# Kernel optimization log

Hardware: AMD Instinct MI355X
Metric: run time of the kernel (lower is better)

The kernel has to match this reference:

```python
import jax, jax.numpy as jnp
import numpy as np

B, S = 2, 2048
DIM_IN, DIM_OUT, NUM_HEADS, DIM_QK = 1024, 128, 16, 128


def setup_inputs() -> dict:
    key = jax.random.key(0)
    k0, k1, k2, k3 = jax.random.split(key, 4)
    x = jax.random.normal(k0, (B, S, DIM_IN), jnp.float32)
    mask = jax.random.bernoulli(k1, 0.1, (B, S))  # True = masked-out token
    # xavier-normal-ish scales (exact init values are irrelevant for correctness)
    std_in = float(np.sqrt(2.0 / (NUM_HEADS * DIM_QK + DIM_IN * DIM_QK)))
    proj_in = jax.random.normal(k2, (DIM_IN, NUM_HEADS, 2 * DIM_QK + DIM_OUT), jnp.float32) * std_in
    v_bias = jnp.zeros((NUM_HEADS, DIM_OUT), jnp.float32)
    std_out = float(np.sqrt(2.0 / (DIM_OUT * DIM_OUT + NUM_HEADS * DIM_OUT)))
    proj_out = jax.random.normal(k3, (NUM_HEADS, DIM_OUT, DIM_OUT), jnp.float32) * std_out
    proj_out_bias = jnp.zeros((DIM_OUT,), jnp.float32)
    return {"x": x, "mask": mask, "proj_in": proj_in, "v_bias": v_bias,
            "proj_out": proj_out, "proj_out_bias": proj_out_bias}


def _rotary(t):
    # t: [z, s, h, d]; GPT-NeoX style rotary as in the torch Rotary module
    d = t.shape[-1]
    half = -(-d // 2)  # ceil(d/2), matches torch.arange(0,-1,-2/d)
    freq_half = 10000.0 ** (jnp.arange(half, dtype=jnp.float32) * (-2.0 / d))
    freq = jnp.concatenate([freq_half, freq_half[: half - d % 2]])  # length d
    pos = jnp.arange(t.shape[1], dtype=jnp.float32)
    ang = pos[:, None] * freq[None, :]             # [s, d]
    cos = jnp.cos(ang)[None, :, None, :]
    sin = jnp.sin(ang)[None, :, None, :]
    x1, x2 = jnp.split(t, 2, axis=-1)
    rot = jnp.concatenate([-x2, x1], axis=-1)
    return t * cos + rot * sin


def _inf_cube(t):
    return t ** 3


def reference(x, mask, proj_in, v_bias, proj_out, proj_out_bias):
    qkv = jnp.einsum('zki,iho->zkho', x, proj_in)
    q, k, v = jnp.split(qkv, [DIM_QK, 2 * DIM_QK], axis=-1)
    q = _rotary(q)
    k = _rotary(k)
    scores = jnp.einsum('zqha,zkha->zqkh', q, k) / jnp.sqrt(jnp.float32(DIM_QK))
    # dual mask: row (query) OR column (key) masked -> -inf
    m = jnp.logical_or(mask[:, :, None, None], mask[:, None, :, None])  # [z,q,k,1]
    scores = jnp.where(m, -jnp.inf, scores)
    attn = jnp.nan_to_num(jax.nn.softmax(scores, axis=2))  # softmax over k; nan rows -> 0
    o = jnp.einsum('zqkh,zkhx->zqhx', attn, v + v_bias[None, None])
    out = jnp.einsum('zqhx,hxy->zqy', _inf_cube(o), proj_out) + proj_out_bias[None, None]
    return _inf_cube(out)
```

## Files before the change

kernel.cpp:

```cpp
#include <hip/hip_runtime.h>
#include <math.h>

#define BZ 2
#define SQ 2048
#define DIN 1024
#define HH 16
#define NT 6144
#define MROWS 4096
#define KOUT 2048
#define KSPLIT 16

typedef unsigned short u16t;
typedef unsigned int u32t;
typedef __attribute__((ext_vector_type(8))) short bf16x8;
typedef __attribute__((ext_vector_type(4))) float f32x4;

__device__ __forceinline__ float cubef(float x) { return x * x * x; }

__device__ __forceinline__ u16t f2bf(float f) {
    u32t b = __float_as_uint(f);
    b += 0x7FFFu + ((b >> 16) & 1u);
    return (u16t)(b >> 16);
}
__device__ __forceinline__ float bf2f(u16t u) { return __uint_as_float(((u32t)u) << 16); }
__device__ __forceinline__ u32t pk2(float a, float b) {
    return (u32t)f2bf(a) | ((u32t)f2bf(b) << 16);
}

#if __has_builtin(__builtin_amdgcn_exp2f)
#define EXP2(x) __builtin_amdgcn_exp2f(x)
#else
#define EXP2(x) exp2f(x)
#endif

__device__ __forceinline__ void load_lds16(const void* g, void* l) {
    __builtin_amdgcn_global_load_lds((const __attribute__((address_space(1))) void*)g,
                                     (__attribute__((address_space(3))) void*)l, 16, 0, 0);
}

__global__ __launch_bounds__(256) void bf16_x(const float* __restrict__ x,
                                              u16t* __restrict__ xb) {
    const size_t idx = ((size_t)blockIdx.x * 256 + threadIdx.x) * 8;
    float4 f0 = *(const float4*)&x[idx];
    float4 f1 = *(const float4*)&x[idx + 4];
    u32t h[4];
    h[0] = pk2(f0.x, f0.y); h[1] = pk2(f0.z, f0.w);
    h[2] = pk2(f1.x, f1.y); h[3] = pk2(f1.z, f1.w);
    *(uint4*)&xb[idx] = *(uint4*)&h[0];
}

__global__ __launch_bounds__(256) void rope_table(float* __restrict__ tab) {
    const int idx = blockIdx.x * 256 + threadIdx.x;
    const int s = idx >> 6, d = idx & 63;
    float f = expf(-0.14391156831212788f * (float)d);
    float sn, cs;
    sincosf((float)s * f, &sn, &cs);
    ((float2*)tab)[idx] = make_float2(cs, sn);
}

__global__ __launch_bounds__(256) void transpose_w(const float* __restrict__ W,
                                                   u16t* __restrict__ Th) {
    __shared__ float tile[64][68];
    const int n0 = blockIdx.x * 64;
    const int k0 = blockIdx.y * 64;
    const int t = threadIdx.x;
    {
        const int r = t >> 4, c = (t & 15) * 4;
        #pragma unroll
        for (int p = 0; p < 4; p++) {
            float4 v = *(const float4*)&W[(size_t)(k0 + r + p * 16) * NT + n0 + c];
            *(float4*)&tile[r + p * 16][c] = v;
        }
    }
    __syncthreads();
    const int nr = t >> 2;
    const int kc = (t & 3) * 16;
    u32t hi[8];
    #pragma unroll
    for (int j = 0; j < 8; j++)
        hi[j] = pk2(tile[kc + 2 * j][nr], tile[kc + 2 * j + 1][nr]);
    size_t ob = (size_t)(n0 + nr) * DIN + k0 + kc;
    *(uint4*)&Th[ob]     = *(uint4*)&hi[0];
    *(uint4*)&Th[ob + 8] = *(uint4*)&hi[4];
}

__global__ __launch_bounds__(256) void transpose_w2(const float* __restrict__ W,
                                                    u16t* __restrict__ Th) {
    __shared__ float tile[64][68];
    const int n0 = blockIdx.x * 64;
    const int k0 = blockIdx.y * 64;
    const int t = threadIdx.x;
    {
        const int r = t >> 4, c = (t & 15) * 4;
        #pragma unroll
        for (int p = 0; p < 4; p++) {
            float4 v = *(const float4*)&W[(size_t)(k0 + r + p * 16) * 128 + n0 + c];
            *(float4*)&tile[r + p * 16][c] = v;
        }
    }
    __syncthreads();
    const int nr = t >> 2;
    const int kc = (t & 3) * 16;
    u32t hi[8];
    #pragma unroll
    for (int j = 0; j < 8; j++)
        hi[j] = pk2(tile[kc + 2 * j][nr], tile[kc + 2 * j + 1][nr]);
    size_t ob = (size_t)(n0 + nr) * KOUT + k0 + kc;
    *(uint4*)&Th[ob]     = *(uint4*)&hi[0];
    *(uint4*)&Th[ob + 8] = *(uint4*)&hi[4];
}

#define QSC 0.12751744f

__global__ __launch_bounds__(256) void gemm_qkv5(const u16t* __restrict__ Ah,
                                                 const u16t* __restrict__ Bh,
                                                 const float* __restrict__ vb,
                                                 const float* __restrict__ ropetab,
                                                 u16t* __restrict__ QB,
                                                 u16t* __restrict__ KB,
                                                 u16t* __restrict__ VTh) {
    __shared__ __align__(16) u16t smem[17408];

    const int t = threadIdx.x;
    const int lane = t & 63, wid = t >> 6;
    const int quad = lane >> 4, l15 = lane & 15;
    const int wm = (wid & 1) * 64;
    const int wn = (wid >> 1) * 64;

    const int f = blockIdx.y * 48 + blockIdx.x;
    const int L = (f & 7) * 192 + (f >> 3);
    const int rect = L / 48, rrem = L - rect * 48;
    const int tileI = (rect & 7) * 6 + rrem % 6;
    const int rowIdx = (rect >> 3) * 8 + rrem / 6;
    const int h = tileI / 3, t3 = tileI - h * 3;
    const int colBase = tileI * 128;
    const int rowBase = rowIdx * 128;
    const int sm = t & 127;
    const int skh = t >> 7;

    f32x4 acc[4][4];
    #pragma unroll
    for (int i = 0; i < 4; i++)
        #pragma unroll
        for (int j = 0; j < 4; j++) acc[i][j] = (f32x4){0.f, 0.f, 0.f, 0.f};

    const u16t* aPtr = Ah + (size_t)(rowBase + sm) * DIN + skh * 16;
    const u16t* bPtr = Bh + (size_t)(colBase + sm) * DIN + skh * 16;
    const int wbase = (wid >> 1) * 2048 + (wid & 1) * 512;

    load_lds16(aPtr,     &smem[wbase]);
    load_lds16(aPtr + 8, &smem[wbase + 1024]);
    load_lds16(bPtr,     &smem[8192 + wbase]);
    load_lds16(bPtr + 8, &smem[8192 + wbase + 1024]);
    __syncthreads();

    for (int it = 0; it < 32; it++) {
        const int buf = it & 1;
        const int ab = buf * 4096, bb_ = 8192 + buf * 4096;
        if (it < 31) {
            const int k0 = (it + 1) * 32;
            const int nab = (buf ^ 1) * 4096, nbb = 8192 + (buf ^ 1) * 4096;
            load_lds16(aPtr + k0,     &smem[nab + wbase]);
            load_lds16(aPtr + k0 + 8, &smem[nab + wbase + 1024]);
            load_lds16(bPtr + k0,     &smem[nbb + wbase]);
            load_lds16(bPtr + k0 + 8, &smem[nbb + wbase + 1024]);
        }
        bf16x8 ah[4], bh[4];
        #pragma unroll
        for (int mt = 0; mt < 4; mt++)
            ah[mt] = *(const bf16x8*)&smem[ab + quad * 1024 + (wm + mt * 16 + l15) * 8];
        #pragma unroll
        for (int nt = 0; nt < 4; nt++)
            bh[nt] = *(const bf16x8*)&smem[bb_ + quad * 1024 + (wn + nt * 16 + l15) * 8];
        #pragma unroll
        for (int mt = 0; mt < 4; mt++)
            #pragma unroll
            for (int nt = 0; nt < 4; nt++)
                acc[mt][nt] = __builtin_amdgcn_mfma_f32_16x16x32_bf16(ah[mt], bh[nt], acc[mt][nt], 0, 0, 0);
        __syncthreads();
    }

    const int z = rowBase >> 11;
    const int s0local = rowBase & 2047;
    const size_t zh = (size_t)(z * 16 + h);
    u16t* tl = smem;

    if (t3 == 2) {
        #pragma unroll
        for (int nt = 0; nt < 4; nt++) {
            float bbv = vb[h * 128 + wn + nt * 16 + l15];
            #pragma unroll
            for (int mt = 0; mt < 4; mt++)
                #pragma unroll
                for (int r = 0; r < 4; r++)
                    tl[(wm + mt * 16 + quad * 4 + r) * 136 + wn + nt * 16 + l15] =
                        f2bf(acc[mt][nt][r] + bbv);
        }
    } else {
        #pragma unroll
        for (int nt = 0; nt < 4; nt++)
            #pragma unroll
            for (int mt = 0; mt < 4; mt++)
                #pragma unroll
                for (int r = 0; r < 4; r++)
                    tl[(wm + mt * 16 + quad * 4 + r) * 136 + wn + nt * 16 + l15] =
                        f2bf(acc[mt][nt][r]);
    }
    __syncthreads();

    if (t3 != 2) {
        u16t* dstQK = (t3 ? KB : QB) + zh * 262144;
        const float sc = t3 ? 1.0f : QSC;
        const int rr = t >> 2;
        const int ch = (t & 3) << 4;
        #pragma unroll
        for (int half = 0; half < 2; half++) {
            const int row = rr + half * 64;
            const int s = s0local + row;
            const u16t* trow = &tl[row * 136];
            uint4 X1  = *(const uint4*)&trow[ch];
            uint4 X1b = *(const uint4*)&trow[ch + 8];
            uint4 X2  = *(const uint4*)&trow[ch + 64];
            uint4 X2b = *(const uint4*)&trow[ch + 72];
            u32t A_[8] = {X1.x, X1.y, X1.z, X1.w, X1b.x, X1b.y, X1b.z, X1b.w};
            u32t B_[8] = {X2.x, X2.y, X2.z, X2.w, X2b.x, X2b.y, X2b.z, X2b.w};
            u32t OA[8], OB[8];
            const float4* tb = (const float4*)&ropetab[(size_t)s * 128 + ch * 2];
            #pragma unroll
            for (int p = 0; p < 8; p++) {
                float4 tt = tb[p];
                float cs0 = tt.x * sc, sn0 = tt.y * sc;
                float cs1 = tt.z * sc, sn1 = tt.w * sc;
                float x1a = bf2f((u16t)(A_[p] & 0xFFFFu)), x1b = bf2f((u16t)(A_[p] >> 16));
                float x2a = bf2f((u16t)(B_[p] & 0xFFFFu)), x2b = bf2f((u16t)(B_[p] >> 16));
                OA[p] = pk2(x1a * cs0 - x2a * sn0, x1b * cs1 - x2b * sn1);
                OB[p] = pk2(x2a * cs0 + x1a * sn0, x2b * cs1 + x1b * sn1);
            }
            u16t* d0 = dstQK + (size_t)s * 128 + ch;
            *(uint4*)d0        = make_uint4(OA[0], OA[1], OA[2], OA[3]);
            *(uint4*)(d0 + 8)  = make_uint4(OA[4], OA[5], OA[6], OA[7]);
            *(uint4*)(d0 + 64) = make_uint4(OB[0], OB[1], OB[2], OB[3]);
            *(uint4*)(d0 + 72) = make_uint4(OB[4], OB[5], OB[6], OB[7]);
        }
    } else {
        u16t* dstV = VTh + zh * 262144 + (size_t)(s0local >> 5) * 4096;
        const int d = t & 127;
        const int g0 = t >> 7;
        #pragma unroll
        for (int gg = 0; gg < 2; gg++) {
            const int g = g0 + 2 * gg;
            const u16t* col = &tl[(g * 32) * 136 + d];
            u32t H[16];
            #pragma unroll
            for (int m = 0; m < 16; m++) {
                u32t lo = col[m * 136];
                u32t hi = col[(m + 16) * 136];
                H[m] = lo | (hi << 16);
            }
            u16t* dv = dstV + (size_t)g * 4096 + d * 32;
            *(uint4*)&dv[0]  = *(uint4*)&H[0];
            *(uint4*)&dv[8]  = *(uint4*)&H[4];
            *(uint4*)&dv[16] = *(uint4*)&H[8];
            *(uint4*)&dv[24] = *(uint4*)&H[12];
        }
    }
}

__global__ __launch_bounds__(256, 2) void attn_kernel8(const u16t* __restrict__ QB,
                                                       const u16t* __restrict__ KB,
                                                       const u16t* __restrict__ VTh,
                                                       const int* __restrict__ mask,
                                                       u16t* __restrict__ O3b) {
    const int blk = blockIdx.x;
    const int qt = blk & 15;
    const int h  = (blk >> 4) & 15;
    const int z  = blk >> 8;
    const int t  = threadIdx.x;
    const int lane = t & 63, wid = t >> 6;
    const int quad = lane >> 4, l15 = lane & 15;

    __shared__ __align__(16) u16t ks[2][32 * 136];
    __shared__ __align__(16) u16t vth[2][128 * 40];
    __shared__ __align__(16) u16t wlb[128 * 40];
    __shared__ int km[2][32];

    const int q0 = qt * 128;
    const size_t zh = (size_t)(z * 16 + h);
    const u16t* qb  = QB  + zh * 262144;
    const u16t* kb  = KB  + zh * 262144;
    const u16t* vhg = VTh + zh * 262144;

    bf16x8 qf[2][4];
    #pragma unroll
    for (int i = 0; i < 2; i++)
        #pragma unroll
        for (int kk = 0; kk < 4; kk++)
            qf[i][kk] = *(const bf16x8*)(qb + (size_t)(q0 + 16 * (2 * wid + i) + l15) * 128 + kk * 32 + quad * 8);

    int4 qm4[2];
    #pragma unroll
    for (int i = 0; i < 2; i++)
        qm4[i] = *(const int4*)&mask[z * SQ + q0 + 16 * (2 * wid + i) + 4 * quad];
    const int qmr[2][4] = {{qm4[0].x, qm4[0].y, qm4[0].z, qm4[0].w},
                           {qm4[1].x, qm4[1].y, qm4[1].z, qm4[1].w}};
    int rowoff[2];
    #pragma unroll
    for (int i = 0; i < 2; i++) rowoff[i] = (16 * (2 * wid + i) + 4 * quad) * 40;

    const int srow = t >> 3, sco = (t & 7) * 16;
    const int sdd = t >> 1, sk0 = (t & 1) * 16;

    uint4 ka, kb2, va, vb2;
    int kmv = 0;
    {
        ka  = *(const uint4*)(kb + t * 16);
        kb2 = *(const uint4*)(kb + t * 16 + 8);
        va  = *(const uint4*)(vhg + t * 16);
        vb2 = *(const uint4*)(vhg + t * 16 + 8);
        if (t < 32) kmv = mask[z * SQ + t];
    }

    f32x4 acc[2][8];
    #pragma unroll
    for (int i = 0; i < 2; i++)
        #pragma unroll
        for (int d = 0; d < 8; d++) acc[i][d] = (f32x4){0.f, 0.f, 0.f, 0.f};
    float dsum[2][4] = {{0.f, 0.f, 0.f, 0.f}, {0.f, 0.f, 0.f, 0.f}};

    for (int it = 0; it < 64; it++) {
        const int buf = it & 1;
        *(uint4*)&ks[buf][srow * 136 + sco]     = ka;
        *(uint4*)&ks[buf][srow * 136 + sco + 8] = kb2;
        *(uint4*)&vth[buf][sdd * 40 + sk0]      = va;
        *(uint4*)&vth[buf][sdd * 40 + sk0 + 8]  = vb2;
        if (t < 32) km[buf][t] = kmv;

        __syncthreads();

        {
            const int ktn = (it < 63) ? (it + 1) * 32 : it * 32;
            const u16t* src = kb + (size_t)ktn * 128 + t * 16;
            ka  = *(const uint4*)(src);
            kb2 = *(const uint4*)(src + 8);
            const u16t* srch = vhg + (size_t)(ktn >> 5) * 4096 + t * 16;
            va  = *(const uint4*)(srch);
            vb2 = *(const uint4*)(srch + 8);
            if (t < 32) kmv = mask[z * SQ + ktn + t];
        }

        f32x4 s4[2][2];
        #pragma unroll
        for (int i = 0; i < 2; i++)
            #pragma unroll
            for (int n = 0; n < 2; n++) s4[i][n] = (f32x4){0.f, 0.f, 0.f, 0.f};
        #pragma unroll
        for (int kk = 0; kk < 4; kk++) {
            bf16x8 kf0 = *(const bf16x8*)&ks[buf][l15 * 136 + kk * 32 + quad * 8];
            bf16x8 kf1 = *(const bf16x8*)&ks[buf][(16 + l15) * 136 + kk * 32 + quad * 8];
            s4[0][0] = __builtin_amdgcn_mfma_f32_16x16x32_bf16(qf[0][kk], kf0, s4[0][0], 0, 0, 0);
            s4[0][1] = __builtin_amdgcn_mfma_f32_16x16x32_bf16(qf[0][kk], kf1, s4[0][1], 0, 0, 0);
            s4[1][0] = __builtin_amdgcn_mfma_f32_16x16x32_bf16(qf[1][kk], kf0, s4[1][0], 0, 0, 0);
            s4[1][1] = __builtin_amdgcn_mfma_f32_16x16x32_bf16(qf[1][kk], kf1, s4[1][1], 0, 0, 0);
        }
        {
            int colm0 = km[buf][l15], colm1 = km[buf][16 + l15];
            #pragma unroll
            for (int i = 0; i < 2; i++)
                #pragma unroll
                for (int r = 0; r < 4; r++) {
                    float w0 = (qmr[i][r] | colm0) ? 0.f : EXP2(s4[i][0][r]);
                    float w1 = (qmr[i][r] | colm1) ? 0.f : EXP2(s4[i][1][r]);
                    dsum[i][r] += w0 + w1;
                    u32t pkw;
                    asm("v_cvt_pk_bf16_f32 %0, %1, %2" : "=v"(pkw) : "v"(w0), "v"(w1));
                    *(u32t*)&wlb[rowoff[i] + r * 40 + 2 * l15] = pkw;
                }
        }
        bf16x8 pa[2];
        #pragma unroll
        for (int i = 0; i < 2; i++)
            pa[i] = *(const bf16x8*)&wlb[(16 * (2 * wid + i) + l15) * 40 + quad * 8];
        #pragma unroll
        for (int dt = 0; dt < 8; dt++) {
            bf16x8 vh = *(const bf16x8*)&vth[buf][(16 * dt + l15) * 40 + quad * 8];
            acc[0][dt] = __builtin_amdgcn_mfma_f32_16x16x32_bf16(pa[0], vh, acc[0][dt], 0, 0, 0);
            acc[1][dt] = __builtin_amdgcn_mfma_f32_16x16x32_bf16(pa[1], vh, acc[1][dt], 0, 0, 0);
        }
    }

    #pragma unroll
    for (int i = 0; i < 2; i++)
        #pragma unroll
        for (int r = 0; r < 4; r++) {
            float v = dsum[i][r];
            v += __shfl_xor(v, 1);
            v += __shfl_xor(v, 2);
            v += __shfl_xor(v, 4);
            v += __shfl_xor(v, 8);
            dsum[i][r] = v;
        }

    #pragma unroll
    for (int i = 0; i < 2; i++)
        #pragma unroll
        for (int r = 0; r < 4; r++) {
            int row = 16 * (2 * wid + i) + 4 * quad + r;
            float inv = dsum[i][r] > 0.f ? 1.f / dsum[i][r] : 0.f;
            u16t* dst = O3b + (size_t)(z * SQ + q0 + row) * KOUT + h * 128;
            #pragma unroll
            for (int dt = 0; dt < 8; dt++)
                dst[16 * dt + l15] = f2bf(cubef(acc[i][dt][r] * inv));
        }
}

__global__ __launch_bounds__(256) void final_gemm3(const u16t* __restrict__ Ab,
                                                   const u16t* __restrict__ Bh,
                                                   float* __restrict__ part) {
    __shared__ __align__(16) u16t as_h[2][4 * 128 * 8];
    __shared__ __align__(16) u16t bs_h[2][4 * 128 * 8];

    const int t = threadIdx.x;
    const int lane = t & 63, wid = t >> 6;
    const int quad = lane >> 4, l15 = lane & 15;
    const int wm = (wid & 1) * 64;
    const int wn = (wid >> 1) * 64;
    const int rowBase = blockIdx.x * 128;
    const int kBase   = blockIdx.y * (KOUT / KSPLIT);
    const int sm = t & 127;
    const int skh = t >> 7;

    f32x4 acc[4][4];
    #pragma unroll
    for (int i = 0; i < 4; i++)
        #pragma unroll
        for (int j = 0; j < 4; j++) acc[i][j] = (f32x4){0.f, 0.f, 0.f, 0.f};

    const u16t* aPtr = Ab + (size_t)(rowBase + sm) * KOUT + kBase + skh * 16;
    const u16t* bPtr = Bh + (size_t)sm * KOUT + kBase + skh * 16;
    const int swoff = (skh * 2) * 1024 + sm * 8;

    uint4 a0 = *(const uint4*)(aPtr);
    uint4 a1 = *(const uint4*)(aPtr + 8);
    uint4 b0 = *(const uint4*)(bPtr);
    uint4 b1 = *(const uint4*)(bPtr + 8);

    const int NIT = (KOUT / KSPLIT) / 32;
    for (int it = 0; it < NIT; it++) {
        const int buf = it & 1;
        *(uint4*)(&as_h[buf][swoff])        = a0;
        *(uint4*)(&as_h[buf][swoff + 1024]) = a1;
        *(uint4*)(&bs_h[buf][swoff])        = b0;
        *(uint4*)(&bs_h[buf][swoff + 1024]) = b1;
        __syncthreads();
        {
            const int k0 = (it < NIT - 1) ? (it + 1) * 32 : it * 32;
            a0 = *(const uint4*)(aPtr + k0);
            a1 = *(const uint4*)(aPtr + k0 + 8);
            b0 = *(const uint4*)(bPtr + k0);
            b1 = *(const uint4*)(bPtr + k0 + 8);
        }
        bf16x8 ah[4], bh[4];
        #pragma unroll
        for (int mt = 0; mt < 4; mt++)
            ah[mt] = *(const bf16x8*)&as_h[buf][quad * 1024 + (wm + mt * 16 + l15) * 8];
        #pragma unroll
        for (int nt = 0; nt < 4; nt++)
            bh[nt] = *(const bf16x8*)&bs_h[buf][quad * 1024 + (wn + nt * 16 + l15) * 8];
        #pragma unroll
        for (int mt = 0; mt < 4; mt++)
            #pragma unroll
            for (int nt = 0; nt < 4; nt++)
                acc[mt][nt] = __builtin_amdgcn_mfma_f32_16x16x32_bf16(ah[mt], bh[nt], acc[mt][nt], 0, 0, 0);
    }

    float* pbase = part + (size_t)blockIdx.y * ((size_t)MROWS * 128);
    #pragma unroll
    for (int mt = 0; mt < 4; mt++)
        #pragma unroll
        for (int nt = 0; nt < 4; nt++) {
            int col = wn + nt * 16 + l15;
            #pragma unroll
            for (int r = 0; r < 4; r++) {
                int row = rowBase + wm + mt * 16 + quad * 4 + r;
                pbase[(size_t)row * 128 + col] = acc[mt][nt][r];
            }
        }
}

__global__ __launch_bounds__(256) void reduce_bias_cube(const float* __restrict__ part,
                                                        const float* __restrict__ bias,
                                                        float* __restrict__ out) {
    const int idx = (blockIdx.x * 256 + threadIdx.x) * 4;
    float4 s = {0.f, 0.f, 0.f, 0.f};
    #pragma unroll
    for (int p = 0; p < KSPLIT; p++) {
        float4 v = *(const float4*)&part[(size_t)p * ((size_t)MROWS * 128) + idx];
        s.x += v.x; s.y += v.y; s.z += v.z; s.w += v.w;
    }
    float4 b = *(const float4*)&bias[idx & 127];
    float4 r;
    r.x = cubef(s.x + b.x);
    r.y = cubef(s.y + b.y);
    r.z = cubef(s.z + b.z);
    r.w = cubef(s.w + b.w);
    *(float4*)&out[idx] = r;
}

extern "C" void kernel_launch(void* const* d_in, const int* in_sizes, int n_in,
                              void* d_out, int out_size, void* d_ws, size_t ws_size,
                              hipStream_t stream) {
    const float* x        = (const float*)d_in[0];
    const int*   mask     = (const int*)d_in[1];
    const float* proj_in  = (const float*)d_in[2];
    const float* v_bias   = (const float*)d_in[3];
    const float* proj_out = (const float*)d_in[4];
    const float* po_bias  = (const float*)d_in[5];
    float* out = (float*)d_out;

    u16t* QB  = (u16t*)d_ws;
    u16t* KB  = QB + (size_t)8388608;
    u16t* VTh = KB + (size_t)8388608;
    u16t* xb  = VTh + (size_t)8388608;
    u16t* O3b = xb + (size_t)4194304;
    u16t* pTh = O3b;
    float* ropetab = (float*)(O3b + (size_t)6291456);
    u16t* WTh = QB;
    float* partials = (float*)(WTh + (size_t)128 * KOUT);

    bf16_x<<<(MROWS * DIN) / (256 * 8), 256, 0, stream>>>(x, xb);
    rope_table<<<(SQ * 64) / 256, 256, 0, stream>>>(ropetab);
    transpose_w<<<dim3(NT / 64, DIN / 64), 256, 0, stream>>>(proj_in, pTh);
    gemm_qkv5<<<dim3(48, MROWS / 128), 256, 0, stream>>>(xb, pTh, v_bias, ropetab, QB, KB, VTh);
    attn_kernel8<<<BZ * HH * (SQ / 128), 256, 0, stream>>>(QB, KB, VTh, mask, O3b);
    transpose_w2<<<dim3(2, KOUT / 64), 256, 0, stream>>>(proj_out, WTh);
    final_gemm3<<<dim3(MROWS / 128, KSPLIT), 256, 0, stream>>>(O3b, WTh, partials);
    reduce_bias_cube<<<(MROWS * 128) / (256 * 4), 256, 0, stream>>>(partials, po_bias, out);
}
```

Measured before the change: 310.4 us.

## Deepen GEMM pipelines to 4-stage async LDS loads, add MFMA priority hints

```diff
diff --git a/kernel.cpp b/kernel.cpp
--- a/kernel.cpp
+++ b/kernel.cpp
@@ -8,7 +8,7 @@
 #define NT 6144
 #define MROWS 4096
 #define KOUT 2048
-#define KSPLIT 16
+#define KSPLIT 8
 
 typedef unsigned short u16t;
 typedef unsigned int u32t;
@@ -112,14 +112,47 @@
 
 #define QSC 0.12751744f
 
-__global__ __launch_bounds__(256) void gemm_qkv5(const u16t* __restrict__ Ah,
-                                                 const u16t* __restrict__ Bh,
-                                                 const float* __restrict__ vb,
-                                                 const float* __restrict__ ropetab,
-                                                 u16t* __restrict__ QB,
-                                                 u16t* __restrict__ KB,
-                                                 u16t* __restrict__ VTh) {
-    __shared__ __align__(16) u16t smem[17408];
+#define GQ_STAGE(TI) do {                                                  \
+    const int _k0 = (TI) * 32;                                             \
+    const int _bb = ((TI) & 3) * 8192;                                     \
+    load_lds16(aPtr + _k0,     &smem[_bb + wbase]);                        \
+    load_lds16(aPtr + _k0 + 8, &smem[_bb + wbase + 1024]);                 \
+    load_lds16(bPtr + _k0,     &smem[_bb + 4096 + wbase]);                 \
+    load_lds16(bPtr + _k0 + 8, &smem[_bb + 4096 + wbase + 1024]);          \
+} while (0)
+
+#define GQ_COMPUTE(TI) do {                                                \
+    const int _bb = ((TI) & 3) * 8192;                                     \
+    bf16x8 ah[4], bh[4];                                                   \
+    _Pragma("unroll")                                                      \
+    for (int mt = 0; mt < 4; mt++)                                         \
+        ah[mt] = *(const bf16x8*)&smem[_bb + quad * 1024 + (wm + mt * 16 + l15) * 8]; \
+    _Pragma("unroll")                                                      \
+    for (int nt = 0; nt < 4; nt++)                                         \
+        bh[nt] = *(const bf16x8*)&smem[_bb + 4096 + quad * 1024 + (wn + nt * 16 + l15) * 8]; \
+    __builtin_amdgcn_s_setprio(1);                                         \
+    _Pragma("unroll")                                                      \
+    for (int mt = 0; mt < 4; mt++)                                         \
+        _Pragma("unroll")                                                  \
+        for (int nt = 0; nt < 4; nt++)                                     \
+            acc[mt][nt] = __builtin_amdgcn_mfma_f32_16x16x32_bf16(ah[mt], bh[nt], acc[mt][nt], 0, 0, 0); \
+    __builtin_amdgcn_s_setprio(0);                                         \
+} while (0)
+
+#define GQ_WAITBAR(N) do {                                                 \
+    asm volatile("s_waitcnt vmcnt(" #N ")" ::: "memory");                  \
+    __builtin_amdgcn_s_barrier();                                          \
+    __builtin_amdgcn_sched_barrier(0);                                     \
+} while (0)
+
+__global__ __launch_bounds__(256, 2) void gemm_qkv6(const u16t* __restrict__ Ah,
+                                                    const u16t* __restrict__ Bh,
+                                                    const float* __restrict__ vb,
+                                                    const float* __restrict__ ropetab,
+                                                    u16t* __restrict__ QB,
+                                                    u16t* __restrict__ KB,
+                                                    u16t* __restrict__ VTh) {
+    __shared__ __align__(16) u16t smem[32768];
 
     const int t = threadIdx.x;
     const int lane = t & 63, wid = t >> 6;
@@ -148,37 +181,18 @@
     const u16t* bPtr = Bh + (size_t)(colBase + sm) * DIN + skh * 16;
     const int wbase = (wid >> 1) * 2048 + (wid & 1) * 512;
 
-    load_lds16(aPtr,     &smem[wbase]);
-    load_lds16(aPtr + 8, &smem[wbase + 1024]);
-    load_lds16(bPtr,     &smem[8192 + wbase]);
-    load_lds16(bPtr + 8, &smem[8192 + wbase + 1024]);
+    GQ_STAGE(0);
+    GQ_STAGE(1);
+    for (int i = 0; i < 30; i++) {
+        GQ_STAGE(i + 2);
+        GQ_WAITBAR(8);
+        GQ_COMPUTE(i);
+    }
+    GQ_WAITBAR(4);
+    GQ_COMPUTE(30);
+    GQ_WAITBAR(0);
+    GQ_COMPUTE(31);
     __syncthreads();
-
-    for (int it = 0; it < 32; it++) {
-        const int buf = it & 1;
-        const int ab = buf * 4096, bb_ = 8192 + buf * 4096;
-        if (it < 31) {
-            const int k0 = (it + 1) * 32;
-            const int nab = (buf ^ 1) * 4096, nbb = 8192 + (buf ^ 1) * 4096;
-            load_lds16(aPtr + k0,     &smem[nab + wbase]);
-            load_lds16(aPtr + k0 + 8, &smem[nab + wbase + 1024]);
-            load_lds16(bPtr + k0,     &smem[nbb + wbase]);
-            load_lds16(bPtr + k0 + 8, &smem[nbb + wbase + 1024]);
-        }
-        bf16x8 ah[4], bh[4];
-        #pragma unroll
-        for (int mt = 0; mt < 4; mt++)
-            ah[mt] = *(const bf16x8*)&smem[ab + quad * 1024 + (wm + mt * 16 + l15) * 8];
-        #pragma unroll
-        for (int nt = 0; nt < 4; nt++)
-            bh[nt] = *(const bf16x8*)&smem[bb_ + quad * 1024 + (wn + nt * 16 + l15) * 8];
-        #pragma unroll
-        for (int mt = 0; mt < 4; mt++)
-            #pragma unroll
-            for (int nt = 0; nt < 4; nt++)
-                acc[mt][nt] = __builtin_amdgcn_mfma_f32_16x16x32_bf16(ah[mt], bh[nt], acc[mt][nt], 0, 0, 0);
-        __syncthreads();
-    }
 
     const int z = rowBase >> 11;
     const int s0local = rowBase & 2047;
@@ -266,7 +280,7 @@
     }
 }
 
-__global__ __launch_bounds__(256, 2) void attn_kernel8(const u16t* __restrict__ QB,
+__global__ __launch_bounds__(256, 2) void attn_kernel9(const u16t* __restrict__ QB,
                                                        const u16t* __restrict__ KB,
                                                        const u16t* __restrict__ VTh,
                                                        const int* __restrict__ mask,
@@ -353,6 +367,7 @@
         for (int i = 0; i < 2; i++)
             #pragma unroll
             for (int n = 0; n < 2; n++) s4[i][n] = (f32x4){0.f, 0.f, 0.f, 0.f};
+        __builtin_amdgcn_s_setprio(1);
         #pragma unroll
         for (int kk = 0; kk < 4; kk++) {
             bf16x8 kf0 = *(const bf16x8*)&ks[buf][l15 * 136 + kk * 32 + quad * 8];
@@ -362,14 +377,15 @@
             s4[1][0] = __builtin_amdgcn_mfma_f32_16x16x32_bf16(qf[1][kk], kf0, s4[1][0], 0, 0, 0);
             s4[1][1] = __builtin_amdgcn_mfma_f32_16x16x32_bf16(qf[1][kk], kf1, s4[1][1], 0, 0, 0);
         }
+        __builtin_amdgcn_s_setprio(0);
         {
             int colm0 = km[buf][l15], colm1 = km[buf][16 + l15];
             #pragma unroll
             for (int i = 0; i < 2; i++)
                 #pragma unroll
                 for (int r = 0; r < 4; r++) {
-                    float w0 = (qmr[i][r] | colm0) ? 0.f : EXP2(s4[i][0][r]);
-                    float w1 = (qmr[i][r] | colm1) ? 0.f : EXP2(s4[i][1][r]);
+                    float w0 = colm0 ? 0.f : EXP2(s4[i][0][r]);
+                    float w1 = colm1 ? 0.f : EXP2(s4[i][1][r]);
                     dsum[i][r] += w0 + w1;
                     u32t pkw;
                     asm("v_cvt_pk_bf16_f32 %0, %1, %2" : "=v"(pkw) : "v"(w0), "v"(w1));
@@ -380,12 +396,14 @@
         #pragma unroll
         for (int i = 0; i < 2; i++)
             pa[i] = *(const bf16x8*)&wlb[(16 * (2 * wid + i) + l15) * 40 + quad * 8];
+        __builtin_amdgcn_s_setprio(1);
         #pragma unroll
         for (int dt = 0; dt < 8; dt++) {
             bf16x8 vh = *(const bf16x8*)&vth[buf][(16 * dt + l15) * 40 + quad * 8];
             acc[0][dt] = __builtin_amdgcn_mfma_f32_16x16x32_bf16(pa[0], vh, acc[0][dt], 0, 0, 0);
             acc[1][dt] = __builtin_amdgcn_mfma_f32_16x16x32_bf16(pa[1], vh, acc[1][dt], 0, 0, 0);
         }
+        __builtin_amdgcn_s_setprio(0);
     }
 
     #pragma unroll
@@ -405,7 +423,7 @@
         #pragma unroll
         for (int r = 0; r < 4; r++) {
             int row = 16 * (2 * wid + i) + 4 * quad + r;
-            float inv = dsum[i][r] > 0.f ? 1.f / dsum[i][r] : 0.f;
+            float inv = (qmr[i][r] || !(dsum[i][r] > 0.f)) ? 0.f : 1.f / dsum[i][r];
             u16t* dst = O3b + (size_t)(z * SQ + q0 + row) * KOUT + h * 128;
             #pragma unroll
             for (int dt = 0; dt < 8; dt++)
@@ -413,11 +431,10 @@
         }
 }
 
-__global__ __launch_bounds__(256) void final_gemm3(const u16t* __restrict__ Ab,
-                                                   const u16t* __restrict__ Bh,
-                                                   float* __restrict__ part) {
-    __shared__ __align__(16) u16t as_h[2][4 * 128 * 8];
-    __shared__ __align__(16) u16t bs_h[2][4 * 128 * 8];
+__global__ __launch_bounds__(256, 2) void final_gemm4(const u16t* __restrict__ Ab,
+                                                      const u16t* __restrict__ Bh,
+                                                      float* __restrict__ part) {
+    __shared__ __align__(16) u16t smem[32768];
 
     const int t = threadIdx.x;
     const int lane = t & 63, wid = t >> 6;
@@ -437,41 +454,19 @@
 
     const u16t* aPtr = Ab + (size_t)(rowBase + sm) * KOUT + kBase + skh * 16;
     const u16t* bPtr = Bh + (size_t)sm * KOUT + kBase + skh * 16;
-    const int swoff = (skh * 2) * 1024 + sm * 8;
-
-    uint4 a0 = *(const uint4*)(aPtr);
-    uint4 a1 = *(const uint4*)(aPtr + 8);
-    uint4 b0 = *(const uint4*)(bPtr);
-    uint4 b1 = *(const uint4*)(bPtr + 8);
-
-    const int NIT = (KOUT / KSPLIT) / 32;
-    for (int it = 0; it < NIT; it++) {
-        const int buf = it & 1;
-        *(uint4*)(&as_h[buf][swoff])        = a0;
-        *(uint4*)(&as_h[buf][swoff + 1024]) = a1;
-        *(uint4*)(&bs_h[buf][swoff])        = b0;
-        *(uint4*)(&bs_h[buf][swoff + 1024]) = b1;
-        __syncthreads();
-        {
-            const int k0 = (it < NIT - 1) ? (it + 1) * 32 : it * 32;
-            a0 = *(const uint4*)(aPtr + k0);
-            a1 = *(const uint4*)(aPtr + k0 + 8);
-            b0 = *(const uint4*)(bPtr + k0);
-            b1 = *(const uint4*)(bPtr + k0 + 8);
-        }
-        bf16x8 ah[4], bh[4];
-        #pragma unroll
-        for (int mt = 0; mt < 4; mt++)
-            ah[mt] = *(const bf16x8*)&as_h[buf][quad * 1024 + (wm + mt * 16 + l15) * 8];
-        #pragma unroll
-        for (int nt = 0; nt < 4; nt++)
-            bh[nt] = *(const bf16x8*)&bs_h[buf][quad * 1024 + (wn + nt * 16 + l15) * 8];
-        #pragma unroll
-        for (int mt = 0; mt < 4; mt++)
-            #pragma unroll
-            for (int nt = 0; nt < 4; nt++)
-                acc[mt][nt] = __builtin_amdgcn_mfma_f32_16x16x32_bf16(ah[mt], bh[nt], acc[mt][nt], 0, 0, 0);
-    }
+    const int wbase = (wid >> 1) * 2048 + (wid & 1) * 512;
+
+    GQ_STAGE(0);
+    GQ_STAGE(1);
+    for (int i = 0; i < 6; i++) {
+        GQ_STAGE(i + 2);
+        GQ_WAITBAR(8);
+        GQ_COMPUTE(i);
+    }
+    GQ_WAITBAR(4);
+    GQ_COMPUTE(6);
+    GQ_WAITBAR(0);
+    GQ_COMPUTE(7);
 
     float* pbase = part + (size_t)blockIdx.y * ((size_t)MROWS * 128);
     #pragma unroll
@@ -530,9 +525,9 @@
     bf16_x<<<(MROWS * DIN) / (256 * 8), 256, 0, stream>>>(x, xb);
     rope_table<<<(SQ * 64) / 256, 256, 0, stream>>>(ropetab);
     transpose_w<<<dim3(NT / 64, DIN / 64), 256, 0, stream>>>(proj_in, pTh);
-    gemm_qkv5<<<dim3(48, MROWS / 128), 256, 0, stream>>>(xb, pTh, v_bias, ropetab, QB, KB, VTh);
-    attn_kernel8<<<BZ * HH * (SQ / 128), 256, 0, stream>>>(QB, KB, VTh, mask, O3b);
+    gemm_qkv6<<<dim3(48, MROWS / 128), 256, 0, stream>>>(xb, pTh, v_bias, ropetab, QB, KB, VTh);
+    attn_kernel9<<<BZ * HH * (SQ / 128), 256, 0, stream>>>(QB, KB, VTh, mask, O3b);
     transpose_w2<<<dim3(2, KOUT / 64), 256, 0, stream>>>(proj_out, WTh);
-    final_gemm3<<<dim3(MROWS / 128, KSPLIT), 256, 0, stream>>>(O3b, WTh, partials);
+    final_gemm4<<<dim3(MROWS / 128, KSPLIT), 256, 0, stream>>>(O3b, WTh, partials);
     reduce_bias_cube<<<(MROWS * 128) / (256 * 4), 256, 0, stream>>>(partials, po_bias, out);
 }
```

After: 300.6 us. 3.2% less time.
